# Kernel tuning notes

Hardware: AMD Instinct MI355X
Metric: run time of the kernel (lower is better)

The kernel has to match this reference:

```python
import jax, jax.numpy as jnp
import numpy as np

THRESH = 1.0      # snntorch Leaky default threshold
SLOPE = 25.0      # surrogate.fast_sigmoid default slope
BETA = 0.9
ENC_TH = 0.5

# Heaviside spike with fast-sigmoid surrogate gradient (snntorch semantics)
@jax.custom_vjp
def spike_fn(x):
    return (x > 0).astype(x.dtype)

def _spk_fwd(x):
    return (x > 0).astype(x.dtype), x

def _spk_bwd(x, g):
    return (g / (SLOPE * jnp.abs(x) + 1.0) ** 2,)

spike_fn.defvjp(_spk_fwd, _spk_bwd)


def delta_encode(x, threshold):
    # x: [B, T, F] -> spikes [T, B, 2F] (time-major for scan)
    B, T, F = x.shape
    xt = jnp.swapaxes(x, 0, 1)  # [T, B, F]

    def step(ref, cur):
        diff = cur - ref
        on = (diff >= threshold).astype(x.dtype)
        off = (diff <= -threshold).astype(x.dtype)
        mask = jnp.maximum(on, off)
        ref = ref * (1.0 - mask) + cur * mask
        return ref, jnp.concatenate([on, off], axis=-1)

    _, spk = jax.lax.scan(step, x[:, 0, :], xt[1:])  # [T-1, B, 2F]
    zeros = jnp.zeros((1, B, 2 * F), x.dtype)        # t=0 row is all zeros
    return jnp.concatenate([zeros, spk], axis=0)


def _lif(mem, cur):
    # snntorch Leaky, reset_mechanism='subtract'
    reset = jax.lax.stop_gradient((mem - THRESH > 0).astype(mem.dtype))
    mem = BETA * mem + cur - reset * THRESH
    spk = spike_fn(mem - THRESH)
    return spk, mem


def setup_inputs() -> dict:
    key = jax.random.key(0)
    ks = jax.random.split(key, 7)
    B, T, F, H, O = 256, 4096, 16, 128, 2
    x = jax.random.normal(ks[0], (B, T, F), dtype=jnp.float32)
    s1 = 1.0 / np.sqrt(2 * F)
    s2 = 1.0 / np.sqrt(H)
    return {
        "x": x,
        "W1": jax.random.uniform(ks[1], (H, 2 * F), jnp.float32, -s1, s1),
        "b1": jax.random.uniform(ks[2], (H,), jnp.float32, -s1, s1),
        "W2": jax.random.uniform(ks[3], (H, H), jnp.float32, -s2, s2),
        "b2": jax.random.uniform(ks[4], (H,), jnp.float32, -s2, s2),
        "W3": jax.random.uniform(ks[5], (O, H), jnp.float32, -s2, s2),
        "b3": jax.random.uniform(ks[6], (O,), jnp.float32, -s2, s2),
    }


def reference(x, W1, b1, W2, b2, W3, b3):
    spk_in = delta_encode(x, ENC_TH)  # [T, B, 2F]
    B = x.shape[0]
    H = W1.shape[0]
    O = W3.shape[0]
    init = (jnp.zeros((B, H), x.dtype), jnp.zeros((B, H), x.dtype), jnp.zeros((B, O), x.dtype))

    def step(carry, s_t):
        m1, m2, m3 = carry
        spk1, m1 = _lif(m1, s_t @ W1.T + b1)
        spk2, m2 = _lif(m2, spk1 @ W2.T + b2)
        _, m3 = _lif(m3, spk2 @ W3.T + b3)
        return (m1, m2, m3), m3

    _, mem3_rec = jax.lax.scan(step, init, spk_in)
    return mem3_rec  # [T, B, O], matches torch.stack(mem3_rec, dim=0)
```

## Files before the change

kernel.cpp:

```cpp
#include <hip/hip_runtime.h>
#include <cstdint>

#define BB 256
#define TT 4096
#define FDIM 16
#define HH 128
#define CH 64
#define NCH (TT / CH)
#define NPROD 13
#define NTHR 1024

typedef unsigned long long u64;
typedef float f32x2 __attribute__((ext_vector_type(2)));
typedef uint32_t u32x4 __attribute__((ext_vector_type(4)));

__device__ __forceinline__ uint32_t lds_addr32(const void* p) {
  return (uint32_t)(uintptr_t)p;
}
__device__ __forceinline__ f32x2 glb_load_b64(uint32_t voff, const void* base) {
  f32x2 d;
  asm volatile("global_load_dwordx2 %0, %1, %2" : "=v"(d) : "v"(voff), "s"(base));
  return d;
}
__device__ __forceinline__ void ds_write_b128_at(uint32_t addr, u32x4 v) {
  asm volatile("ds_write_b128 %0, %1" ::"v"(addr), "v"(v));
}
#define DSW32(A, D) asm volatile("ds_write_b32 %0, %1" ::"v"(A), "v"(D));
#define DSW64(A, D) asm volatile("ds_write_b64 %0, %1" ::"v"(A), "v"(D));
#define WAIT_VM(N)                                          \
  {                                                         \
    asm volatile("s_waitcnt vmcnt(" #N ")" ::: "memory");   \
    __builtin_amdgcn_sched_barrier(0);                      \
  }
#define WAIT_LGKM(N)                                        \
  {                                                         \
    asm volatile("s_waitcnt lgkmcnt(" #N ")" ::: "memory"); \
    __builtin_amdgcn_sched_barrier(0);                      \
  }
#define DSR64(D, A, OFF) \
  asm volatile("ds_read_b64 %0, %1 offset:" #OFF : "=v"(D) : "v"(A));
#define DSR128(D, A, OFF) \
  asm volatile("ds_read_b128 %0, %1 offset:" #OFF : "=v"(D) : "v"(A));
#define DS_READ_OFF(D, A, OFF) \
  asm volatile("ds_read_b32 %0, %1 offset:" #OFF : "=v"(D) : "v"(A));

__device__ __forceinline__ f32x2 pk_add(f32x2 a, f32x2 b) {
  f32x2 d;
  asm("v_pk_add_f32 %0, %1, %2" : "=v"(d) : "v"(a), "v"(b));
  return d;
}
__device__ __forceinline__ u64 rfl64(u64 x) {
  uint32_t lo = (uint32_t)__builtin_amdgcn_readfirstlane((int)(uint32_t)x);
  uint32_t hi = (uint32_t)__builtin_amdgcn_readfirstlane((int)(uint32_t)(x >> 32));
  return ((u64)hi << 32) | lo;
}
__device__ __forceinline__ uint32_t mbcnt64(u64 m) {
  uint32_t r = __builtin_amdgcn_mbcnt_lo((uint32_t)m, 0u);
  return __builtin_amdgcn_mbcnt_hi((uint32_t)(m >> 32), r);
}
__device__ __forceinline__ float wave_red_add63(float v) {
#define DPP_ADD(c)                                                             \
  v += __int_as_float(                                                         \
      __builtin_amdgcn_update_dpp(0, __float_as_int(v), c, 0xF, 0xF, true))
  DPP_ADD(0x111);
  DPP_ADD(0x112);
  DPP_ADD(0x114);
  DPP_ADD(0x118);
  DPP_ADD(0x142);
  DPP_ADD(0x143);
#undef DPP_ADD
  return v;
}

__global__ __launch_bounds__(64) void snn_prep(const float* __restrict__ W1,
                                               const float* __restrict__ W2,
                                               f32x2* __restrict__ w1t,
                                               f32x2* __restrict__ w2t) {
  const int l = threadIdx.x;
  for (int j = 0; j < 64; ++j)
    w1t[j * 64 + l] = (j < 32) ? f32x2{W1[l * 32 + j], W1[(64 + l) * 32 + j]}
                               : f32x2{0.f, 0.f};
  for (int j = 0; j < 129; ++j)
    w2t[j * 64 + l] = (j < 128) ? f32x2{W2[l * 128 + j], W2[(64 + l) * 128 + j]}
                                : f32x2{0.f, 0.f};
}

__global__ __launch_bounds__(64) void snn_encode(const float* __restrict__ x,
                                                 uint32_t* __restrict__ masks) {
  __shared__ float tile[2][4][64][16];
  const int lane = threadIdx.x;
  const int sub = lane >> 4;
  const int f = lane & 15;
  const int b0 = blockIdx.x * 4;
  float ref = x[(size_t)(b0 + sub) * (TT * FDIM) + f];

  const float4* xv = (const float4*)x;
  float4 ld[16];
#define K1_ISSUE(G)                                                           \
  _Pragma("unroll") for (int k = 0; k < 16; ++k) {                            \
    int idx4 = k * 64 + lane;                                                 \
    int bl = idx4 >> 8;                                                       \
    int r = idx4 & 255;                                                       \
    ld[k] = xv[(size_t)(b0 + bl) * (TT * 4) + (size_t)(G) * 256 + r];         \
  }
#define K1_WRITE(BUF)                                                         \
  _Pragma("unroll") for (int k = 0; k < 16; ++k) {                            \
    int idx4 = k * 64 + lane;                                                 \
    int bl = idx4 >> 8;                                                       \
    int r = idx4 & 255;                                                       \
    ((float4*)&tile[BUF][bl][0][0])[r] = ld[k];                               \
  }
#define CHUNK_ISSUE(ARR, A)                                                   \
  {                                                                           \
    DS_READ_OFF(ARR[0], A, 0);                                                \
    DS_READ_OFF(ARR[1], A, 64);                                               \
    DS_READ_OFF(ARR[2], A, 128);                                              \
    DS_READ_OFF(ARR[3], A, 192);                                              \
    DS_READ_OFF(ARR[4], A, 256);                                              \
    DS_READ_OFF(ARR[5], A, 320);                                              \
    DS_READ_OFF(ARR[6], A, 384);                                              \
    DS_READ_OFF(ARR[7], A, 448);                                              \
  }
#define PROC8(ARR, TBASE)                                                     \
  _Pragma("unroll") for (int i = 0; i < 8; ++i) {                             \
    float cur = ARR[i];                                                       \
    float diff = cur - ref;                                                   \
    bool onb = diff >= 0.5f;                                                  \
    bool offb = diff <= -0.5f;                                                \
    u64 bon = __ballot(onb);                                                  \
    u64 boff = __ballot(offb);                                                \
    ref = (onb || offb) ? cur : ref;                                          \
    if (f == 0) {                                                             \
      uint32_t mk = (uint32_t)((bon >> (sub * 16)) & 0xFFFFull) |             \
                    ((uint32_t)((boff >> (sub * 16)) & 0xFFFFull) << 16);     \
      masks[(size_t)(b0 + sub) * TT + ((TBASE) + i)] = mk;                    \
    }                                                                         \
  }

  const uint32_t tbase =
      lds_addr32(&tile[0][0][0][0]) + (uint32_t)sub * 4096u + (uint32_t)f * 4u;

  K1_ISSUE(0);
  K1_WRITE(0);
  WAIT_LGKM(0);
  for (int g = 0; g < TT / 64; ++g) {
    if (g + 1 < TT / 64) K1_ISSUE(g + 1);
    const int buf = g & 1;
    const uint32_t caddr = tbase + (uint32_t)buf * 16384u;
    float va[8], vb[8];
    CHUNK_ISSUE(va, caddr);
#pragma unroll
    for (int c = 0; c < 8; ++c) {
      if (c < 7) {
        uint32_t an = caddr + (uint32_t)(c + 1) * 512u;
        if (c & 1) {
          CHUNK_ISSUE(va, an);
        } else {
          CHUNK_ISSUE(vb, an);
        }
        WAIT_LGKM(8);
      } else {
        WAIT_LGKM(0);
      }
      if (c & 1) {
        PROC8(vb, g * 64 + c * 8);
      } else {
        PROC8(va, g * 64 + c * 8);
      }
    }
    if (g + 1 < TT / 64) {
      K1_WRITE((g + 1) & 1);
      WAIT_LGKM(0);
    }
  }
#undef PROC8
#undef CHUNK_ISSUE
#undef K1_WRITE
#undef K1_ISSUE
}

__global__ __launch_bounds__(NTHR, 1) void snn_core15(
    const uint32_t* __restrict__ masks, const f32x2* __restrict__ w1t,
    const f32x2* __restrict__ w2t, const float* __restrict__ b1,
    const float* __restrict__ b2, const float* __restrict__ W3,
    const float* __restrict__ b3, float* __restrict__ out) {
  __shared__ f32x2 C1b[2][CH][64];
  __shared__ f32x2 C2b[2][CH][64];
  __shared__ f32x2 C3b[2][CH];
  __shared__ __align__(16) u64 S2[2][CH][2];
  __shared__ __align__(16) uint32_t IDX0[2][CH][16];
  __shared__ __align__(16) uint32_t IDX1[2][CH][16];
  __shared__ __align__(16) u64 S1R[2][CH][2];

  const int tid = threadIdx.x;
  const int lane = tid & 63;
  const int wv = tid >> 6;
  const int b = blockIdx.x;
  const uint32_t lane8 = (uint32_t)lane * 8u;

  const f32x2 bias1 = {b1[lane], b1[64 + lane]};
  const f32x2 bias2 = {b2[lane], b2[64 + lane]};
  const float w30a = W3[lane], w30b = W3[64 + lane];
  const float w31a = W3[128 + lane], w31b = W3[192 + lane];
  const float b30 = b3[0], b31 = b3[1];
  float m1a = 0.f, m1b = 0.f, m2a = 0.f, m2b = 0.f, m3x = 0.f, m3y = 0.f;
  float2* outv = (float2*)out;
  const uint32_t* mrow = masks + (size_t)b * TT;

  const uint32_t idx0b = lds_addr32(&IDX0[0][0][0]);
  const uint32_t idx1b = lds_addr32(&IDX1[0][0][0]);
  const uint32_t s1rb = lds_addr32(&S1R[0][0][0]);

#define IDX0_BUILD(KK)                                                        \
  if ((KK) >= 0 && (KK) < NCH) {                                              \
    const uint32_t p0_ = idx0b + (uint32_t)(((KK) & 1) * (CH * 64));          \
    uint32_t mm_ = mrow[(KK)*CH + lane];                                      \
    _Pragma("unroll") for (int i = 0; i < CH; ++i) {                          \
      uint32_t mk_ = (uint32_t)__builtin_amdgcn_readlane((int)mm_, i);        \
      uint32_t ib_ = p0_ + (uint32_t)(i * 64);                                \
      if (lane < 16) { DSW32(ib_ + (uint32_t)lane * 4u, 16384u); }            \
      uint32_t r_ = __builtin_amdgcn_mbcnt_lo(mk_, 0u);                       \
      bool bt_ = (((u64)mk_ >> lane) & 1) != 0;                               \
      if (bt_) { DSW32(ib_ + r_ * 4u, (uint32_t)lane << 9); }                 \
    }                                                                         \
    WAIT_LGKM(0);                                                             \
  }

  __syncthreads();
  if (wv == 15) IDX0_BUILD(0);

#define LD4(BUF, Q, S0, W)                                                    \
  BUF[S0] = glb_load_b64(Q.x + lane8, W);                                     \
  BUF[S0 + 1] = glb_load_b64(Q.y + lane8, W);                                 \
  BUF[S0 + 2] = glb_load_b64(Q.z + lane8, W);                                 \
  BUF[S0 + 3] = glb_load_b64(Q.w + lane8, W);
#define ISSUE_C1(TASK)                                                        \
  {                                                                           \
    uint32_t ib_ = idx0b + (uint32_t)((k & 1) * (CH * 64)) + (uint32_t)((TASK)*64); \
    u32x4 q0_, q1_, q2_, q3_;                                                 \
    DSR128(q0_, ib_, 0);                                                      \
    DSR128(q1_, ib_, 16);                                                     \
    DSR128(q2_, ib_, 32);                                                     \
    DSR128(q3_, ib_, 48);                                                     \
    WAIT_LGKM(0);                                                             \
    LD4(B1, q0_, 0, w1t) LD4(B1, q1_, 4, w1t)                                 \
    LD4(B1, q2_, 8, w1t) LD4(B1, q3_, 12, w1t)                                \
  }
#define CONSUME_C1(TASK)                                                      \
  {                                                                           \
    f32x2 c_ = {0.f, 0.f};                                                    \
    _Pragma("unroll") for (int s = 0; s < 16; ++s) c_ = pk_add(c_, B1[s]);    \
    c_ = pk_add(c_, bias1);                                                   \
    C1b[k & 1][(TASK)][lane] = c_;                                            \
  }
#define ISSUE_C2(TASK, C2Q)                                                   \
  {                                                                           \
    uint32_t ib_ = idx1b + (uint32_t)(((C2Q)&1) * (CH * 64)) +                \
                   (uint32_t)((TASK)*64);                                     \
    uint32_t rq_ = s1rb + (uint32_t)(((C2Q)&1) * (CH * 16)) +                 \
                   (uint32_t)((TASK)*16);                                     \
    u32x4 q0_, q1_, q2_, q3_, qr_;                                            \
    DSR128(q0_, ib_, 0);                                                      \
    DSR128(q1_, ib_, 16);                                                     \
    DSR128(q2_, ib_, 32);                                                     \
    DSR128(q3_, ib_, 48);                                                     \
    DSR128(qr_, rq_, 0);                                                      \
    WAIT_LGKM(0);                                                             \
    LD4(B2, q0_, 0, w2t) LD4(B2, q1_, 4, w2t)                                 \
    LD4(B2, q2_, 8, w2t) LD4(B2, q3_, 12, w2t)                                \
    taP = (u64)qr_.x | ((u64)qr_.y << 32);                                    \
    tbP = (u64)qr_.z | ((u64)qr_.w << 32);                                    \
  }
#define CONSUME_C2(TASK, C2Q)                                                 \
  {                                                                           \
    f32x2 c_ = {0.f, 0.f};                                                    \
    _Pragma("unroll") for (int s = 0; s < 16; ++s) c_ = pk_add(c_, B2[s]);    \
    while (taP) {     \
      uint32_t j_ = (uint32_t)__builtin_ctzll(taP);                           \
      taP &= taP - 1;                                                         \
      f32x2 tw_ = glb_load_b64((j_ << 9) + lane8, w2t);                       \
      WAIT_VM(0);                                                             \
      c_ = pk_add(c_, tw_);                                                   \
    }                                                                         \
    while (tbP) {                                                             \
      uint32_t j_ = 64u + (uint32_t)__builtin_ctzll(tbP);                     \
      tbP &= tbP - 1;                                                         \
      f32x2 tw_ = glb_load_b64((j_ << 9) + lane8, w2t);                       \
      WAIT_VM(0);                                                             \
      c_ = pk_add(c_, tw_);                                                   \
    }                                                                         \
    c_ = pk_add(c_, bias2);                                                   \
    C2b[(C2Q)&1][(TASK)][lane] = c_;                                          \
  }
#define C3_TASK(T3)                                                           \
  {                                                                           \
    int c3_ = k - 4;                                                          \
    if (c3_ >= 0 && c3_ < NCH) {                                              \
      u64 a_ = rfl64(S2[c3_ & 1][(T3)][0]);                                   \
      u64 b_ = rfl64(S2[c3_ & 1][(T3)][1]);                                   \
      float v0 = (((a_ >> lane) & 1) ? w30a : 0.f) +                          \
                 (((b_ >> lane) & 1) ? w30b : 0.f);                           \
      float v1 = (((a_ >> lane) & 1) ? w31a : 0.f) +                          \
                 (((b_ >> lane) & 1) ? w31b : 0.f);                           \
      float r0 = wave_red_add63(v0);                                          \
      float r1 = wave_red_add63(v1);                                          \
      if (lane == 63) C3b[c3_ & 1][(T3)] = f32x2{r0 + b30, r1 + b31};         \
    }                                                                         \
  }

#define ISSUE16_512(ARR, A)                                                   \
  {                                                                           \
    DSR64(ARR[0], A, 0);     DSR64(ARR[1], A, 512);                           \
    DSR64(ARR[2], A, 1024);  DSR64(ARR[3], A, 1536);                          \
    DSR64(ARR[4], A, 2048);  DSR64(ARR[5], A, 2560);                          \
    DSR64(ARR[6], A, 3072);  DSR64(ARR[7], A, 3584);                          \
    DSR64(ARR[8], A, 4096);  DSR64(ARR[9], A, 4608);                          \
    DSR64(ARR[10], A, 5120); DSR64(ARR[11], A, 5632);                         \
    DSR64(ARR[12], A, 6144); DSR64(ARR[13], A, 6656);                         \
    DSR64(ARR[14], A, 7168); DSR64(ARR[15], A, 7680);                         \
  }
#define ISSUE16_8(ARR, A)                                                     \
  {                                                                           \
    DSR64(ARR[0], A, 0);   DSR64(ARR[1], A, 8);                               \
    DSR64(ARR[2], A, 16);  DSR64(ARR[3], A, 24);                              \
    DSR64(ARR[4], A, 32);  DSR64(ARR[5], A, 40);                              \
    DSR64(ARR[6], A, 48);  DSR64(ARR[7], A, 56);                              \
    DSR64(ARR[8], A, 64);  DSR64(ARR[9], A, 72);                              \
    DSR64(ARR[10], A, 80); DSR64(ARR[11], A, 88);                             \
    DSR64(ARR[12], A, 96); DSR64(ARR[13], A, 104);                            \
    DSR64(ARR[14], A, 112); DSR64(ARR[15], A, 120);                           \
  }
#define SCAN1_G(P1, PR, TB)                                                   \
  _Pragma("unroll") for (int i = 0; i < 16; ++i) {                            \
    f32x2 cv_ = arr_[i];                                                      \
    float n0_ = __fadd_rn(__fmul_rn(0.9f, m1a), cv_.x);                       \
    float n1_ = __fadd_rn(__fmul_rn(0.9f, m1b), cv_.y);                       \
    m1a = (m1a > 1.f) ? (n0_ - 1.f) : n0_;                                    \
    m1b = (m1b > 1.f) ? (n1_ - 1.f) : n1_;                                    \
    u64 s0_ = __ballot(m1a > 1.f);                                            \
    u64 s1_ = __ballot(m1b > 1.f);                                            \
    uint32_t ib_ = (P1) + (uint32_t)(((TB) + i) * 64);                        \
    if (lane < 16) { DSW32(ib_ + (uint32_t)lane * 4u, 65536u); }              \
    uint32_t r0_ = mbcnt64(s0_);                                              \
    bool b0_ = ((s0_ >> lane) & 1) != 0;                                      \
    if (b0_ && r0_ < 16u) { DSW32(ib_ + r0_ * 4u, (uint32_t)lane << 9); }     \
    uint32_t c0_ = (uint32_t)__builtin_popcountll(s0_);                       \
    uint32_t r1_ = c0_ + mbcnt64(s1_);                                        \
    bool b1_ = ((s1_ >> lane) & 1) != 0;                                      \
    if (b1_ && r1_ < 16u) {                                                   \
      DSW32(ib_ + r1_ * 4u, (uint32_t)(64 + lane) << 9);                      \
    }                                                                         \
    u64 e0_ = __ballot(b0_ && r0_ >= 16u);                                    \
    u64 e1_ = __ballot(b1_ && r1_ >= 16u);                                    \
    if (lane == 0) {                                                          \
      DSW64((PR) + (uint32_t)(((TB) + i) * 16), e0_);                         \
      DSW64((PR) + (uint32_t)(((TB) + i) * 16 + 8), e1_);                     \
    }                                                                         \
  }
#define SCAN1(CHK)                                                            \
  {                                                                           \
    const int par_ = (CHK) & 1;                                               \
    const uint32_t rb_ = lds_addr32(&C1b[par_][0][0]) + lane8;                \
    const uint32_t p1_ = idx1b + (uint32_t)(par_ * (CH * 64));                \
    const uint32_t pr_ = s1rb + (uint32_t)(par_ * (CH * 16));                 \
    f32x2 arr_[16];                                                           \
    ISSUE16_512(arr_, rb_);                                                   \
    WAIT_LGKM(0);                                                             \
    SCAN1_G(p1_, pr_, 0)                                                      \
    ISSUE16_512(arr_, (rb_ + 8192u));                                         \
    WAIT_LGKM(0);                                                             \
    SCAN1_G(p1_, pr_, 16)                                                     \
    ISSUE16_512(arr_, (rb_ + 16384u));                                        \
    WAIT_LGKM(0);                                                             \
    SCAN1_G(p1_, pr_, 32)                                                     \
    ISSUE16_512(arr_, (rb_ + 24576u));                                        \
    WAIT_LGKM(0);                                                             \
    SCAN1_G(p1_, pr_, 48)                                                     \
    WAIT_LGKM(0);                                                             \
  }
#define SCAN2_G(SB, TB)                                                       \
  _Pragma("unroll") for (int i = 0; i < 16; ++i) {                            \
    f32x2 cv_ = arr_[i];                                                      \
    float n0_ = __fadd_rn(__fmul_rn(0.9f, m2a), cv_.x);                       \
    float n1_ = __fadd_rn(__fmul_rn(0.9f, m2b), cv_.y);                       \
    m2a = (m2a > 1.f) ? (n0_ - 1.f) : n0_;                                    \
    m2b = (m2b > 1.f) ? (n1_ - 1.f) : n1_;                                    \
    u64 s0_ = __ballot(m2a > 1.f);                                            \
    u64 s1_ = __ballot(m2b > 1.f);                                            \
    if (lane == 0)                                                            \
      ds_write_b128_at((SB) + (uint32_t)(((TB) + i) * 16),                    \
                       u32x4{(uint32_t)s0_, (uint32_t)(s0_ >> 32),            \
                             (uint32_t)s1_, (uint32_t)(s1_ >> 32)});          \
  }
#define SCAN2(CHK)                                                            \
  {                                                                           \
    const int par_ = (CHK) & 1;                                               \
    const uint32_t rb_ = lds_addr32(&C2b[par_][0][0]) + lane8;                \
    const uint32_t sb_ = lds_addr32(&S2[par_][0][0]);                         \
    f32x2 arr_[16];                                                           \
    ISSUE16_512(arr_, rb_);                                                   \
    WAIT_LGKM(0);                                                             \
    SCAN2_G(sb_, 0)                                                           \
    ISSUE16_512(arr_, (rb_ + 8192u));                                         \
    WAIT_LGKM(0);                                                             \
    SCAN2_G(sb_, 16)                                                          \
    ISSUE16_512(arr_, (rb_ + 16384u));                                        \
    WAIT_LGKM(0);                                                             \
    SCAN2_G(sb_, 32)                                                          \
    ISSUE16_512(arr_, (rb_ + 24576u));                                        \
    WAIT_LGKM(0);                                                             \
    SCAN2_G(sb_, 48)                                                          \
    WAIT_LGKM(0);                                                             \
  }
#define SCAN3_G(CHK, TB)                                                      \
  _Pragma("unroll") for (int i = 0; i < 16; ++i) {                            \
    f32x2 c3_ = arr_[i];                                                      \
    float e0_ = __fadd_rn(__fmul_rn(0.9f, m3x), c3_.x);                       \
    float e1_ = __fadd_rn(__fmul_rn(0.9f, m3y), c3_.y);                       \
    m3x = (m3x > 1.f) ? (e0_ - 1.f) : e0_;                                    \
    m3y = (m3y > 1.f) ? (e1_ - 1.f) : e1_;                                    \
    if (lane == 0)                                                            \
      outv[(size_t)((CHK)*CH + (TB) + i) * BB + b] = make_float2(m3x, m3y);   \
  }
#define SCAN3(CHK)                                                            \
  {                                                                           \
    const int par_ = (CHK) & 1;                                               \
    const uint32_t cb_ = lds_addr32(&C3b[par_][0]);                           \
    f32x2 arr_[16];                                                           \
    ISSUE16_8(arr_, cb_);                                                     \
    WAIT_LGKM(0);                                                             \
    SCAN3_G(CHK, 0)                                                           \
    ISSUE16_8(arr_, (cb_ + 128u));                                            \
    WAIT_LGKM(0);                                                             \
    SCAN3_G(CHK, 16)                                                          \
    ISSUE16_8(arr_, (cb_ + 256u));                                            \
    WAIT_LGKM(0);                                                             \
    SCAN3_G(CHK, 32)                                                          \
    ISSUE16_8(arr_, (cb_ + 384u));                                            \
    WAIT_LGKM(0);                                                             \
    SCAN3_G(CHK, 48)                                                          \
  }

  for (int k = 0; k < NCH + 5; ++k) {
    __syncthreads();
    if (wv < NPROD) {
      const bool doC1 = (k < NCH);
      const int c2q = k - 2;
      const bool doC2 = (c2q >= 0) && (c2q < NCH);
      f32x2 B1[16], B2[16];
      u64 taP = 0, tbP = 0;
      if (doC1 && doC2) {
        int p = wv;
        ISSUE_C1(p);
        for (;;) {
          ISSUE_C2(p, c2q);
          WAIT_VM(16);
          CONSUME_C1(p);
          int pn = p + NPROD;
          if (pn < CH) {
            ISSUE_C1(pn);
            WAIT_VM(16);
          } else {
            WAIT_VM(0);
          }
          CONSUME_C2(p, c2q);
          if (pn >= CH) break;
          p = pn;
        }
      } else if (doC1) {
        for (int p = wv; p < CH; p += NPROD) {
          ISSUE_C1(p);
          WAIT_VM(0);
          CONSUME_C1(p);
        }
      } else if (doC2) {
        for (int p = wv; p < CH; p += NPROD) {
          ISSUE_C2(p, c2q);
          WAIT_VM(0);
          CONSUME_C2(p, c2q);
        }
      }
      for (int t3 = wv; t3 < CH; t3 += NPROD) {
        C3_TASK(t3);
      }
    } else if (wv == 13) {
      if (k >= 1 && k - 1 < NCH) SCAN1(k - 1);
    } else if (wv == 14) {
      if (k >= 3 && k - 3 < NCH) SCAN2(k - 3);
      if (k >= 5 && k - 5 < NCH) SCAN3(k - 5);
    } else {
      IDX0_BUILD(k + 1);
    }
  }
#undef SCAN3
#undef SCAN3_G
#undef SCAN2
#undef SCAN2_G
#undef SCAN1
#undef SCAN1_G
#undef ISSUE16_8
#undef ISSUE16_512
#undef C3_TASK
#undef CONSUME_C2
#undef ISSUE_C2
#undef CONSUME_C1
#undef ISSUE_C1
#undef LD4
#undef IDX0_BUILD
}

extern "C" void kernel_launch(void* const* d_in, const int* in_sizes, int n_in,
                              void* d_out, int out_size, void* d_ws,
                              size_t ws_size, hipStream_t stream) {
  const float* x = (const float*)d_in[0];
  const float* W1 = (const float*)d_in[1];
  const float* b1 = (const float*)d_in[2];
  const float* W2 = (const float*)d_in[3];
  const float* b2 = (const float*)d_in[4];
  const float* W3 = (const float*)d_in[5];
  const float* b3 = (const float*)d_in[6];
  float* out = (float*)d_out;

  uint32_t* masks = (uint32_t*)d_ws;
  char* wbase = (char*)d_ws + (size_t)BB * TT * 4;
  f32x2* w1t = (f32x2*)wbase;
  f32x2* w2t = (f32x2*)(wbase + 32768);

  snn_prep<<<1, 64, 0, stream>>>(W1, W2, w1t, w2t);
  snn_encode<<<BB / 4, 64, 0, stream>>>(x, masks);
  snn_core15<<<BB, NTHR, 0, stream>>>(masks, w1t, w2t, b1, b2, W3, b3, out);
}
```

Before: 1.306 ms.

## Stage W2 table in LDS and halve chunk length to fit shared memory

Copies the transposed W2 table (129x64 f32x2) into shared memory once per block, so layer-2 gathers and the residual loops read LDS instead of global memory. The chunk size drops from 64 to 32 timesteps so the extra LDS fits, and the scan loops are shortened to match. Because C2 now runs synchronously on LDS, the software pipeline that overlapped C1 and C2 global loads is simplified. The cost is twice as many chunk iterations and block barriers, plus a one-time LDS fill per block.

Measured after the change: 1.166 ms (median of 2 runs). 1.12x faster.

```diff
diff --git a/kernel.cpp b/kernel.cpp
--- a/kernel.cpp
+++ b/kernel.cpp
@@ -5,7 +5,7 @@
 #define TT 4096
 #define FDIM 16
 #define HH 128
-#define CH 64
+#define CH 32
 #define NCH (TT / CH)
 #define NPROD 13
 #define NTHR 1024
@@ -179,11 +179,12 @@
 #undef K1_ISSUE
 }
 
-__global__ __launch_bounds__(NTHR, 1) void snn_core15(
+__global__ __launch_bounds__(NTHR, 1) void snn_core17(
     const uint32_t* __restrict__ masks, const f32x2* __restrict__ w1t,
     const f32x2* __restrict__ w2t, const float* __restrict__ b1,
     const float* __restrict__ b2, const float* __restrict__ W3,
     const float* __restrict__ b3, float* __restrict__ out) {
+  __shared__ __align__(16) f32x2 W2L[129 * 64];
   __shared__ f32x2 C1b[2][CH][64];
   __shared__ f32x2 C2b[2][CH][64];
   __shared__ f32x2 C3b[2][CH];
@@ -197,6 +198,8 @@
   const int wv = tid >> 6;
   const int b = blockIdx.x;
   const uint32_t lane8 = (uint32_t)lane * 8u;
+
+  for (int i = tid; i < 129 * 64; i += NTHR) W2L[i] = w2t[i];
 
   const f32x2 bias1 = {b1[lane], b1[64 + lane]};
   const f32x2 bias2 = {b2[lane], b2[64 + lane]};
@@ -210,11 +213,12 @@
   const uint32_t idx0b = lds_addr32(&IDX0[0][0][0]);
   const uint32_t idx1b = lds_addr32(&IDX1[0][0][0]);
   const uint32_t s1rb = lds_addr32(&S1R[0][0][0]);
+  const uint32_t w2lb = lds_addr32(&W2L[0]);
 
 #define IDX0_BUILD(KK)                                                        \
   if ((KK) >= 0 && (KK) < NCH) {                                              \
     const uint32_t p0_ = idx0b + (uint32_t)(((KK) & 1) * (CH * 64));          \
-    uint32_t mm_ = mrow[(KK)*CH + lane];                                      \
+    uint32_t mm_ = mrow[(KK)*CH + (lane & 31)];                               \
     _Pragma("unroll") for (int i = 0; i < CH; ++i) {                          \
       uint32_t mk_ = (uint32_t)__builtin_amdgcn_readlane((int)mm_, i);        \
       uint32_t ib_ = p0_ + (uint32_t)(i * 64);                                \
@@ -229,36 +233,39 @@
   __syncthreads();
   if (wv == 15) IDX0_BUILD(0);
 
-#define LD4(BUF, Q, S0, W)                                                    \
+#define LD4G(BUF, Q, S0, W)                                                   \
   BUF[S0] = glb_load_b64(Q.x + lane8, W);                                     \
   BUF[S0 + 1] = glb_load_b64(Q.y + lane8, W);                                 \
   BUF[S0 + 2] = glb_load_b64(Q.z + lane8, W);                                 \
   BUF[S0 + 3] = glb_load_b64(Q.w + lane8, W);
-#define ISSUE_C1(TASK)                                                        \
-  {                                                                           \
-    uint32_t ib_ = idx0b + (uint32_t)((k & 1) * (CH * 64)) + (uint32_t)((TASK)*64); \
+#define LD4L(BUF, Q, S0)                                                      \
+  DSR64(BUF[S0], w2lb + Q.x + lane8, 0);                                      \
+  DSR64(BUF[S0 + 1], w2lb + Q.y + lane8, 0);                                  \
+  DSR64(BUF[S0 + 2], w2lb + Q.z + lane8, 0);                                  \
+  DSR64(BUF[S0 + 3], w2lb + Q.w + lane8, 0);
+#define ISSUE_C1(P)                                                           \
+  {                                                                           \
+    uint32_t ib_ = idx0b + (uint32_t)((k & 1) * (CH * 64)) + (uint32_t)((P)*64); \
     u32x4 q0_, q1_, q2_, q3_;                                                 \
     DSR128(q0_, ib_, 0);                                                      \
     DSR128(q1_, ib_, 16);                                                     \
     DSR128(q2_, ib_, 32);                                                     \
     DSR128(q3_, ib_, 48);                                                     \
     WAIT_LGKM(0);                                                             \
-    LD4(B1, q0_, 0, w1t) LD4(B1, q1_, 4, w1t)                                 \
-    LD4(B1, q2_, 8, w1t) LD4(B1, q3_, 12, w1t)                                \
-  }
-#define CONSUME_C1(TASK)                                                      \
+    LD4G(B1, q0_, 0, w1t) LD4G(B1, q1_, 4, w1t)                               \
+    LD4G(B1, q2_, 8, w1t) LD4G(B1, q3_, 12, w1t)                              \
+  }
+#define CONSUME_C1(P)                                                         \
   {                                                                           \
     f32x2 c_ = {0.f, 0.f};                                                    \
     _Pragma("unroll") for (int s = 0; s < 16; ++s) c_ = pk_add(c_, B1[s]);    \
     c_ = pk_add(c_, bias1);                                                   \
-    C1b[k & 1][(TASK)][lane] = c_;                                            \
-  }
-#define ISSUE_C2(TASK, C2Q)                                                   \
-  {                                                                           \
-    uint32_t ib_ = idx1b + (uint32_t)(((C2Q)&1) * (CH * 64)) +                \
-                   (uint32_t)((TASK)*64);                                     \
-    uint32_t rq_ = s1rb + (uint32_t)(((C2Q)&1) * (CH * 16)) +                 \
-                   (uint32_t)((TASK)*16);                                     \
+    C1b[k & 1][(P)][lane] = c_;                                               \
+  }
+#define C2_TASK_LDS(P, C2Q)                                                   \
+  {                                                                           \
+    uint32_t ib_ = idx1b + (uint32_t)(((C2Q)&1) * (CH * 64)) + (uint32_t)((P)*64); \
+    uint32_t rq_ = s1rb + (uint32_t)(((C2Q)&1) * (CH * 16)) + (uint32_t)((P)*16); \
     u32x4 q0_, q1_, q2_, q3_, qr_;                                            \
     DSR128(q0_, ib_, 0);                                                      \
     DSR128(q1_, ib_, 16);                                                     \
@@ -266,31 +273,30 @@
     DSR128(q3_, ib_, 48);                                                     \
     DSR128(qr_, rq_, 0);                                                      \
     WAIT_LGKM(0);                                                             \
-    LD4(B2, q0_, 0, w2t) LD4(B2, q1_, 4, w2t)                                 \
-    LD4(B2, q2_, 8, w2t) LD4(B2, q3_, 12, w2t)                                \
-    taP = (u64)qr_.x | ((u64)qr_.y << 32);                                    \
-    tbP = (u64)qr_.z | ((u64)qr_.w << 32);                                    \
-  }
-#define CONSUME_C2(TASK, C2Q)                                                 \
-  {                                                                           \
+    LD4L(B2, q0_, 0) LD4L(B2, q1_, 4) LD4L(B2, q2_, 8) LD4L(B2, q3_, 12)      \
+    u64 ta_ = (u64)qr_.x | ((u64)qr_.y << 32);                                \
+    u64 tb_ = (u64)qr_.z | ((u64)qr_.w << 32);                                \
+    WAIT_LGKM(0);                                                             \
     f32x2 c_ = {0.f, 0.f};                                                    \
     _Pragma("unroll") for (int s = 0; s < 16; ++s) c_ = pk_add(c_, B2[s]);    \
-    while (taP) {     \
-      uint32_t j_ = (uint32_t)__builtin_ctzll(taP);                           \
-      taP &= taP - 1;                                                         \
-      f32x2 tw_ = glb_load_b64((j_ << 9) + lane8, w2t);                       \
-      WAIT_VM(0);                                                             \
+    while (ta_) {                      \
+      uint32_t j_ = (uint32_t)__builtin_ctzll(ta_);                           \
+      ta_ &= ta_ - 1;                                                         \
+      f32x2 tw_;                                                              \
+      DSR64(tw_, w2lb + (j_ << 9) + lane8, 0);                                \
+      WAIT_LGKM(0);                                                           \
       c_ = pk_add(c_, tw_);                                                   \
     }                                                                         \
-    while (tbP) {                                                             \
-      uint32_t j_ = 64u + (uint32_t)__builtin_ctzll(tbP);                     \
-      tbP &= tbP - 1;                                                         \
-      f32x2 tw_ = glb_load_b64((j_ << 9) + lane8, w2t);                       \
-      WAIT_VM(0);                                                             \
+    while (tb_) {                                                             \
+      uint32_t j_ = 64u + (uint32_t)__builtin_ctzll(tb_);                     \
+      tb_ &= tb_ - 1;                                                         \
+      f32x2 tw_;                                                              \
+      DSR64(tw_, w2lb + (j_ << 9) + lane8, 0);                                \
+      WAIT_LGKM(0);                                                           \
       c_ = pk_add(c_, tw_);                                                   \
     }                                                                         \
     c_ = pk_add(c_, bias2);                                                   \
-    C2b[(C2Q)&1][(TASK)][lane] = c_;                                          \
+    C2b[(C2Q)&1][(P)][lane] = c_;                                             \
   }
 #define C3_TASK(T3)                                                           \
   {                                                                           \
@@ -370,12 +376,6 @@
     ISSUE16_512(arr_, (rb_ + 8192u));                                         \
     WAIT_LGKM(0);                                                             \
     SCAN1_G(p1_, pr_, 16)                                                     \
-    ISSUE16_512(arr_, (rb_ + 16384u));                                        \
-    WAIT_LGKM(0);                                                             \
-    SCAN1_G(p1_, pr_, 32)                                                     \
-    ISSUE16_512(arr_, (rb_ + 24576u));                                        \
-    WAIT_LGKM(0);                                                             \
-    SCAN1_G(p1_, pr_, 48)                                                     \
     WAIT_LGKM(0);                                                             \
   }
 #define SCAN2_G(SB, TB)                                                       \
@@ -404,12 +404,6 @@
     ISSUE16_512(arr_, (rb_ + 8192u));                                         \
     WAIT_LGKM(0);                                                             \
     SCAN2_G(sb_, 16)                                                          \
-    ISSUE16_512(arr_, (rb_ + 16384u));                                        \
-    WAIT_LGKM(0);                                                             \
-    SCAN2_G(sb_, 32)                                                          \
-    ISSUE16_512(arr_, (rb_ + 24576u));                                        \
-    WAIT_LGKM(0);                                                             \
-    SCAN2_G(sb_, 48)                                                          \
     WAIT_LGKM(0);                                                             \
   }
 #define SCAN3_G(CHK, TB)                                                      \
@@ -433,12 +427,6 @@
     ISSUE16_8(arr_, (cb_ + 128u));                                            \
     WAIT_LGKM(0);                                                             \
     SCAN3_G(CHK, 16)                                                          \
-    ISSUE16_8(arr_, (cb_ + 256u));                                            \
-    WAIT_LGKM(0);                                                             \
-    SCAN3_G(CHK, 32)                                                          \
-    ISSUE16_8(arr_, (cb_ + 384u));                                            \
-    WAIT_LGKM(0);                                                             \
-    SCAN3_G(CHK, 48)                                                          \
   }
 
   for (int k = 0; k < NCH + 5; ++k) {
@@ -448,24 +436,12 @@
       const int c2q = k - 2;
       const bool doC2 = (c2q >= 0) && (c2q < NCH);
       f32x2 B1[16], B2[16];
-      u64 taP = 0, tbP = 0;
       if (doC1 && doC2) {
-        int p = wv;
-        ISSUE_C1(p);
-        for (;;) {
-          ISSUE_C2(p, c2q);
-          WAIT_VM(16);
+        for (int p = wv; p < CH; p += NPROD) {
+          ISSUE_C1(p);
+          C2_TASK_LDS(p, c2q);
+          WAIT_VM(0);
           CONSUME_C1(p);
-          int pn = p + NPROD;
-          if (pn < CH) {
-            ISSUE_C1(pn);
-            WAIT_VM(16);
-          } else {
-            WAIT_VM(0);
-          }
-          CONSUME_C2(p, c2q);
-          if (pn >= CH) break;
-          p = pn;
         }
       } else if (doC1) {
         for (int p = wv; p < CH; p += NPROD) {
@@ -475,9 +451,7 @@
         }
       } else if (doC2) {
         for (int p = wv; p < CH; p += NPROD) {
-          ISSUE_C2(p, c2q);
-          WAIT_VM(0);
-          CONSUME_C2(p, c2q);
+          C2_TASK_LDS(p, c2q);
         }
       }
       for (int t3 = wv; t3 < CH; t3 += NPROD) {
@@ -501,11 +475,11 @@
 #undef ISSUE16_8
 #undef ISSUE16_512
 #undef C3_TASK
-#undef CONSUME_C2
-#undef ISSUE_C2
+#undef C2_TASK_LDS
 #undef CONSUME_C1
 #undef ISSUE_C1
-#undef LD4
+#undef LD4L
+#undef LD4G
 #undef IDX0_BUILD
 }
 
@@ -528,5 +502,5 @@
 
   snn_prep<<<1, 64, 0, stream>>>(W1, W2, w1t, w2t);
   snn_encode<<<BB / 4, 64, 0, stream>>>(x, masks);
-  snn_core15<<<BB, NTHR, 0, stream>>>(masks, w1t, w2t, b1, b2, W3, b3, out);
-}
+  snn_core17<<<BB, NTHR, 0, stream>>>(masks, w1t, w2t, b1, b2, W3, b3, out);
+}
```
